# Kernel optimization log

Hardware: AMD Instinct MI355X
Metric: run time of the kernel (lower is better)

## Reference

```python
import jax, jax.numpy as jnp
import numpy as np
from jax import lax

EPS = 1e-5

def _conv(x, w, b, pad):
    y = lax.conv_general_dilated(x, w, (1, 1), [(pad, pad), (pad, pad)],
                                 dimension_numbers=('NCHW', 'OIHW', 'NCHW'))
    return y + b[None, :, None, None]

def _bn(x, g, b, m, v):
    # eval-mode BatchNorm2d with running stats
    scale = g * lax.rsqrt(v + EPS)
    return x * scale[None, :, None, None] + (b - m * scale)[None, :, None, None]

def setup_inputs() -> dict:
    key = jax.random.key(0)
    ks = jax.random.split(key, 16)
    B, C, H, W = 16, 64, 128, 128
    C2 = 2 * C
    d = {}
    d['x'] = jax.random.normal(ks[0], (B, C, H, W), jnp.float32)
    # fc1: Conv2d(C,C,3,p=1) + BN(C)
    d['fc1_w'] = jax.random.normal(ks[1], (C, C, 3, 3), jnp.float32) * 0.05
    d['fc1_b'] = jax.random.normal(ks[2], (C,), jnp.float32) * 0.05
    d['bn1_g'] = jnp.ones((C,), jnp.float32)
    d['bn1_b'] = jnp.zeros((C,), jnp.float32)
    d['bn1_m'] = jax.random.normal(ks[3], (C,), jnp.float32) * 0.05
    d['bn1_v'] = jax.random.uniform(ks[4], (C,), jnp.float32) * 0.5 + 0.5
    # graph_conv.nn: Conv2d(2C,2C,1) + BN(2C) + GELU
    d['gc_w'] = jax.random.normal(ks[5], (C2, C2, 1, 1), jnp.float32) * 0.05
    d['gc_b'] = jax.random.normal(ks[6], (C2,), jnp.float32) * 0.05
    d['bng_g'] = jnp.ones((C2,), jnp.float32)
    d['bng_b'] = jnp.zeros((C2,), jnp.float32)
    d['bng_m'] = jax.random.normal(ks[7], (C2,), jnp.float32) * 0.05
    d['bng_v'] = jax.random.uniform(ks[8], (C2,), jnp.float32) * 0.5 + 0.5
    # fc2: Conv2d(2C,C,3,p=1) + BN(C)
    d['fc2_w'] = jax.random.normal(ks[9], (C, C2, 3, 3), jnp.float32) * 0.05
    d['fc2_b'] = jax.random.normal(ks[10], (C,), jnp.float32) * 0.05
    d['bn2_g'] = jnp.ones((C,), jnp.float32)
    d['bn2_b'] = jnp.zeros((C,), jnp.float32)
    d['bn2_m'] = jax.random.normal(ks[11], (C,), jnp.float32) * 0.05
    d['bn2_v'] = jax.random.uniform(ks[12], (C,), jnp.float32) * 0.5 + 0.5
    return d

def reference(x, fc1_w, fc1_b, bn1_g, bn1_b, bn1_m, bn1_v,
              gc_w, gc_b, bng_g, bng_b, bng_m, bng_v,
              fc2_w, fc2_b, bn2_g, bn2_b, bn2_m, bn2_v):
    # fc1
    h = _bn(_conv(x, fc1_w, fc1_b, 1), bn1_g, bn1_b, bn1_m, bn1_v)
    # MRConv4dSP: strided self-attention over superpatch tokens
    sel = h[:, :, ::4, ::4]                          # [B,C,h4,w4]
    B, C, h4, w4 = sel.shape
    q = sel.reshape(B, C, h4 * w4).transpose(0, 2, 1)  # [B,N,C]
    scale = C ** (-0.5)
    att = jax.nn.softmax(jnp.einsum('bnc,bmc->bnm', q, q) * scale, axis=-1)
    o = jnp.einsum('bnm,bmc->bnc', att, q)           # [B,N,C]
    o = o.transpose(0, 2, 1).reshape(B, C, h4, w4)
    o = jnp.repeat(jnp.repeat(o, 4, axis=2), 4, axis=3)
    g = jnp.concatenate([h, o], axis=1)              # [B,2C,H,W]
    g = jax.nn.gelu(_bn(_conv(g, gc_w, gc_b, 0), bng_g, bng_b, bng_m, bng_v),
                    approximate=False)
    # fc2 + residual (drop_path=0 -> identity)
    y = _bn(_conv(g, fc2_w, fc2_b, 1), bn2_g, bn2_b, bn2_m, bn2_v)
    return y + x
```

## Files before the change

kernel.cpp:

```cpp
#include <hip/hip_runtime.h>
#include <math.h>

#define EPSV 1e-5f

typedef __bf16 bf16;
using bf16x8 = __attribute__((ext_vector_type(8))) __bf16;
using bf16x4 = __attribute__((ext_vector_type(4))) __bf16;
using bf16x2 = __attribute__((ext_vector_type(2))) __bf16;
using f32x4  = __attribute__((ext_vector_type(4))) float;

static __device__ __forceinline__ f32x4 mfma16(bf16x8 a, bf16x8 b, f32x4 c) {
    return __builtin_amdgcn_mfma_f32_16x16x32_bf16(a, b, c, 0, 0, 0);
}
static __device__ __forceinline__ f32x4 zero4() {
    f32x4 z = {0.f, 0.f, 0.f, 0.f};
    return z;
}
static __device__ __forceinline__ bf16x8 zero8() {
    bf16x8 z = {(bf16)0.f,(bf16)0.f,(bf16)0.f,(bf16)0.f,
                (bf16)0.f,(bf16)0.f,(bf16)0.f,(bf16)0.f};
    return z;
}

static __device__ __forceinline__ float gelu_f(float v) {
    float z = fabsf(v) * 0.70710678118f;
    float t = __builtin_amdgcn_rcpf(1.f + 0.3275911f * z);
    float poly = t * (0.254829592f + t * (-0.284496736f + t * (1.421413741f +
                 t * (-1.453152027f + t * 1.061405429f))));
    float e = __expf(-z * z);
    float erfv = copysignf(1.f - poly * e, v);
    return 0.5f * v * (1.f + erfv);
}

template<int CIN>
__global__ __launch_bounds__(256) void prep_conv_w(const float* __restrict__ w,
                                                   bf16* __restrict__ wt)
{
    int t = blockIdx.x * 256 + threadIdx.x;
    if (t >= 64 * CIN) return;
    int cout = t / CIN, ci = t - cout * CIN;
    int cci = ci >> 5, lg = (ci >> 3) & 3, j = ci & 7;
#pragma unroll
    for (int kgt = 0; kgt < 9; ++kgt) {
        float v = w[(size_t)t * 9 + kgt];
        wt[((((size_t)kgt * (CIN >> 5) + cci) * 4 + lg) * 64 + cout) * 8 + j] = (bf16)v;
    }
}

__global__ __launch_bounds__(256) void prep_1x1_w(const float* __restrict__ w,
                                                  bf16* __restrict__ wt)
{
    int t = blockIdx.x * 256 + threadIdx.x;
    int cout = t >> 7, ci = t & 127;
    int ks = ci >> 5, lg = (ci >> 3) & 3, j = ci & 7;
    wt[(((size_t)(ks * 4 + lg) * 128) + cout) * 8 + j] = (bf16)w[t];
}

__global__ __launch_bounds__(256) void cvt_x_nhwc(const float* __restrict__ x,
                                                  bf16* __restrict__ xb)
{
    __shared__ float t_lds[64 * 68];
    const int bx = blockIdx.x;
    const int b  = blockIdx.y;
    const int y  = bx >> 1, x0 = (bx & 1) * 64;
    const int tid = threadIdx.x;

    for (int f = tid; f < 64 * 16; f += 256) {
        int c = f >> 4, xu = f & 15;
        float4 v = *(const float4*)&x[((size_t)(b * 64 + c) << 14) + (y << 7) + x0 + xu * 4];
        t_lds[(xu * 4 + 0) * 68 + c] = v.x;
        t_lds[(xu * 4 + 1) * 68 + c] = v.y;
        t_lds[(xu * 4 + 2) * 68 + c] = v.z;
        t_lds[(xu * 4 + 3) * 68 + c] = v.w;
    }
    __syncthreads();
    for (int f = tid; f < 64 * 8; f += 256) {
        int xx = f >> 3, cu = f & 7;
        const float* p = &t_lds[xx * 68 + cu * 8];
        bf16x8 v;
#pragma unroll
        for (int j = 0; j < 8; ++j) v[j] = (bf16)p[j];
        *(bf16x8*)&xb[((size_t)((b * 128 + y) * 128) + x0 + xx) * 64 + cu * 8] = v;
    }
}

template<int CIN, int OUTMODE>
__global__ __launch_bounds__(512, 4) void conv3x3_mfma(
    const bf16* __restrict__ in, const bf16* __restrict__ wt,
    const float* __restrict__ bias,
    const float* __restrict__ bg, const float* __restrict__ bb,
    const float* __restrict__ bm, const float* __restrict__ bv,
    const float* __restrict__ resid, void* __restrict__ outp)
{
    constexpr int NC = CIN >> 5;
    __shared__ bf16 in_lds[10 * 34 * 40];

    const int tile = blockIdx.x;
    const int b    = blockIdx.y;
    const int x0 = (tile & 3) * 32;
    const int y0 = (tile >> 2) * 8;
    const int tid  = threadIdx.x;
    const int wid  = tid >> 6;
    const int lane = tid & 63;
    const int lix  = lane & 15, lg = lane >> 4;

    f32x4 acc[4][2];
#pragma unroll
    for (int i = 0; i < 4; ++i)
#pragma unroll
        for (int j = 0; j < 2; ++j) acc[i][j] = zero4();

    auto load_chunk = [&](int cci, bf16x8* pre) {
#pragma unroll
        for (int k = 0; k < 2; ++k) {
            int f = tid + k * 512;
            int u = f & 3, pix = f >> 2;
            int iy = pix / 34, ix = pix - iy * 34;
            int gy = y0 + iy - 1, gx = x0 + ix - 1;
            bf16x8 v = zero8();
            if ((unsigned)gy < 128u && (unsigned)gx < 128u)
                v = *(const bf16x8*)&in[((size_t)((b * 128 + gy) * 128 + gx)) * CIN + cci * 32 + u * 8];
            pre[k] = v;
        }
        {
            int f = 1024 + tid;
            int u = f & 3, pix = f >> 2;
            int iy = pix / 34, ix = pix - iy * 34;
            int gy = y0 + iy - 1, gx = x0 + ix - 1;
            bf16x8 v = zero8();
            if (tid < 336 && (unsigned)gy < 128u && (unsigned)gx < 128u)
                v = *(const bf16x8*)&in[((size_t)((b * 128 + gy) * 128 + gx)) * CIN + cci * 32 + u * 8];
            pre[2] = v;
        }
    };
    auto write_chunk = [&](const bf16x8* pre) {
#pragma unroll
        for (int k = 0; k < 2; ++k) {
            int f = tid + k * 512;
            int u = f & 3, pix = f >> 2;
            *(bf16x8*)&in_lds[pix * 40 + u * 8] = pre[k];
        }
        if (tid < 336) {
            int f = 1024 + tid;
            int u = f & 3, pix = f >> 2;
            *(bf16x8*)&in_lds[pix * 40 + u * 8] = pre[2];
        }
    };
    auto load_af = [&](int kgt, int cci, bf16x8* af) {
#pragma unroll
        for (int mi = 0; mi < 4; ++mi)
            af[mi] = *(const bf16x8*)&wt[((((size_t)kgt * NC + cci) * 4 + lg) * 64 + mi * 16 + lix) * 8];
    };
    auto compute = [&](int cci) {
        bf16x8 afA[4], afB[4];
        load_af(0, cci, afA);
#pragma unroll
        for (int kgt = 0; kgt < 9; ++kgt) {
            const int kg = kgt / 3, t = kgt % 3;
            bf16x8* cur = (kgt & 1) ? afB : afA;
            bf16x8* nxt = (kgt & 1) ? afA : afB;
            if (kgt < 8) load_af(kgt + 1, cci, nxt);
#pragma unroll
            for (int nj = 0; nj < 2; ++nj) {
                bf16x8 bfr = *(const bf16x8*)&in_lds[((wid + kg) * 34 + lix + t + nj * 16) * 40 + lg * 8];
#pragma unroll
                for (int mi = 0; mi < 4; ++mi)
                    acc[mi][nj] = mfma16(cur[mi], bfr, acc[mi][nj]);
            }
        }
    };

    bf16x8 preA[3], preB[3];
    load_chunk(0, preA);
#pragma unroll 1
    for (int cci = 0; cci < NC; cci += 2) {
        __syncthreads();
        write_chunk(preA);
        if (cci + 1 < NC) load_chunk(cci + 1, preB);
        __syncthreads();
        compute(cci);
        __syncthreads();
        write_chunk(preB);
        if (cci + 2 < NC) load_chunk(cci + 2, preA);
        __syncthreads();
        compute(cci + 1);
    }

    if (OUTMODE == 0) {
        bf16* out  = (bf16*)outp;
        bf16* stg  = in_lds;
#pragma unroll 1
        for (int p = 0; p < 2; ++p) {
            __syncthreads();
            if ((wid >> 2) == p) {
                int gyloc = wid & 3;
#pragma unroll
                for (int mi = 0; mi < 4; ++mi) {
                    float A[4], Bc[4];
#pragma unroll
                    for (int r = 0; r < 4; ++r) {
                        int c = mi * 16 + lg * 4 + r;
                        float s = bg[c] * rsqrtf(bv[c] + EPSV);
                        A[r]  = s;
                        Bc[r] = bias[c] * s + bb[c] - bm[c] * s;
                    }
#pragma unroll
                    for (int nj = 0; nj < 2; ++nj) {
                        int px = nj * 16 + lix;
                        bf16x4 vv;
#pragma unroll
                        for (int r = 0; r < 4; ++r)
                            vv[r] = (bf16)(acc[mi][nj][r] * A[r] + Bc[r]);
                        *(bf16x4*)&stg[(gyloc * 32 + px) * 68 + mi * 16 + lg * 4] = vv;
                    }
                }
            }
            __syncthreads();
#pragma unroll
            for (int k = 0; k < 2; ++k) {
                int idx = k * 512 + tid;
                int gyloc = idx >> 8, rem = idx & 255;
                int px = rem >> 3, cu = rem & 7;
                int gy = y0 + p * 4 + gyloc;
                bf16x8 v = *(const bf16x8*)&stg[(gyloc * 32 + px) * 68 + cu * 8];
                *(bf16x8*)&out[((size_t)((b * 128 + gy) * 128) + x0 + px) * 64 + cu * 8] = v;
            }
        }
    } else {
        float* out = (float*)outp;
        const int gy = y0 + wid;
#pragma unroll
        for (int mi = 0; mi < 4; ++mi) {
            float A[4], Bc[4];
#pragma unroll
            for (int r = 0; r < 4; ++r) {
                int c = mi * 16 + lg * 4 + r;
                float s = bg[c] * rsqrtf(bv[c] + EPSV);
                A[r]  = s;
                Bc[r] = bias[c] * s + bb[c] - bm[c] * s;
            }
#pragma unroll
            for (int nj = 0; nj < 2; ++nj) {
                int px = x0 + nj * 16 + lix;
#pragma unroll
                for (int r = 0; r < 4; ++r) {
                    int c = mi * 16 + lg * 4 + r;
                    size_t oi = ((size_t)(b * 64 + c) << 14) + (gy << 7) + px;
                    out[oi] = acc[mi][nj][r] * A[r] + Bc[r] + resid[oi];
                }
            }
        }
    }
}

__global__ __launch_bounds__(256) void gather_q(const bf16* __restrict__ h,
                                                bf16* __restrict__ q)
{
    int t = blockIdx.x * 256 + threadIdx.x;
    int cu = t & 7, n = (t >> 3) & 1023, b = t >> 13;
    int y = (n >> 5) << 2, x = (n & 31) << 2;
    bf16x8 v = *(const bf16x8*)&h[((size_t)((b * 128 + y) * 128 + x)) * 64 + cu * 8];
    *(bf16x8*)&q[((size_t)(b * 1024 + n)) * 64 + cu * 8] = v;
}

__global__ __launch_bounds__(256) void attn_fused(const bf16* __restrict__ q,
                                                  bf16* __restrict__ o)
{
    __shared__ bf16 qn[64 * 72];
    __shared__ bf16 kn[128 * 72];
    __shared__ bf16 vt[64 * 136];
    __shared__ bf16 pl[4][16 * 136];
    __shared__ __align__(16) float fac[4][16];
    const int n0 = blockIdx.x * 64, b = blockIdx.y;
    const int tid = threadIdx.x, w = tid >> 6, lane = tid & 63;
    const int lix = lane & 15, lg = lane >> 4;
    const bf16* qb = q + ((size_t)b << 16);

    for (int f = tid; f < 512; f += 256) {
        int row = f >> 3, cu = f & 7;
        *(bf16x8*)&qn[row * 72 + cu * 8] =
            *(const bf16x8*)&qb[(size_t)(n0 + row) * 64 + cu * 8];
    }

    float m_run = -3.0e38f, l_run = 0.f;
    f32x4 oacc[4];
#pragma unroll
    for (int ct = 0; ct < 4; ++ct) oacc[ct] = zero4();

    for (int mt = 0; mt < 1024; mt += 128) {
        __syncthreads();
        for (int f = tid; f < 1024; f += 256) {
            int row = f >> 3, cu = f & 7;
            *(bf16x8*)&kn[row * 72 + cu * 8] =
                *(const bf16x8*)&qb[(size_t)(mt + row) * 64 + cu * 8];
        }
        for (int f = tid; f < 512; f += 256) {
            int mp = f >> 3, cu = f & 7;
            int m = mp * 2;
            bf16x8 a = *(const bf16x8*)&qb[(size_t)(mt + m) * 64 + cu * 8];
            bf16x8 c = *(const bf16x8*)&qb[(size_t)(mt + m + 1) * 64 + cu * 8];
#pragma unroll
            for (int j = 0; j < 8; ++j) {
                bf16x2 pr = {a[j], c[j]};
                *(bf16x2*)&vt[(cu * 8 + j) * 136 + m] = pr;
            }
        }
        __syncthreads();

        bf16x8 bq0 = *(const bf16x8*)&qn[(w * 16 + lix) * 72 + lg * 8];
        bf16x8 bq1 = *(const bf16x8*)&qn[(w * 16 + lix) * 72 + 32 + lg * 8];

        f32x4 s[8];
#pragma unroll
        for (int t = 0; t < 8; ++t) {
            bf16x8 a0 = *(const bf16x8*)&kn[(t * 16 + lix) * 72 + lg * 8];
            bf16x8 a1 = *(const bf16x8*)&kn[(t * 16 + lix) * 72 + 32 + lg * 8];
            s[t] = mfma16(a0, bq0, zero4());
            s[t] = mfma16(a1, bq1, s[t]);
        }

        float mx = -3.0e38f;
#pragma unroll
        for (int t = 0; t < 8; ++t)
#pragma unroll
            for (int r = 0; r < 4; ++r) { s[t][r] *= 0.125f; mx = fmaxf(mx, s[t][r]); }
        mx = fmaxf(mx, __shfl_xor(mx, 16));
        mx = fmaxf(mx, __shfl_xor(mx, 32));
        float m_new = fmaxf(m_run, mx);
        float alpha = __expf(m_run - m_new);

        float psum = 0.f;
#pragma unroll
        for (int t = 0; t < 8; ++t) {
            float p0 = __expf(s[t][0] - m_new), p1 = __expf(s[t][1] - m_new);
            float p2 = __expf(s[t][2] - m_new), p3 = __expf(s[t][3] - m_new);
            psum += (p0 + p1) + (p2 + p3);
            bf16x2 v01 = {(bf16)p0, (bf16)p1};
            bf16x2 v23 = {(bf16)p2, (bf16)p3};
            *(bf16x2*)&pl[w][lix * 136 + t * 16 + lg * 4]     = v01;
            *(bf16x2*)&pl[w][lix * 136 + t * 16 + lg * 4 + 2] = v23;
        }
        psum += __shfl_xor(psum, 16);
        psum += __shfl_xor(psum, 32);
        l_run = l_run * alpha + psum;
        m_run = m_new;
        if (lg == 0) fac[w][lix] = alpha;

        float4 a4 = *(const float4*)&fac[w][lg * 4];
        float aa[4] = {a4.x, a4.y, a4.z, a4.w};
#pragma unroll
        for (int ct = 0; ct < 4; ++ct)
#pragma unroll
            for (int r = 0; r < 4; ++r) oacc[ct][r] *= aa[r];

#pragma unroll
        for (int kk = 0; kk < 4; ++kk) {
            bf16x8 pa = *(const bf16x8*)&pl[w][lix * 136 + kk * 32 + lg * 8];
#pragma unroll
            for (int ct = 0; ct < 4; ++ct) {
                bf16x8 bv = *(const bf16x8*)&vt[(ct * 16 + lix) * 136 + kk * 32 + lg * 8];
                oacc[ct] = mfma16(pa, bv, oacc[ct]);
            }
        }
    }

    if (lg == 0) fac[w][lix] = l_run;
    float4 l4 = *(const float4*)&fac[w][lg * 4];
    float ll[4] = {1.f / l4.x, 1.f / l4.y, 1.f / l4.z, 1.f / l4.w};
#pragma unroll
    for (int ct = 0; ct < 4; ++ct)
#pragma unroll
        for (int r = 0; r < 4; ++r) {
            int n = n0 + w * 16 + lg * 4 + r;
            int c = ct * 16 + lix;
            o[((size_t)(b * 1024 + n)) * 64 + c] = (bf16)(oacc[ct][r] * ll[r]);
        }
}

__global__ __launch_bounds__(256) void conv1x1_mfma(
    const bf16* __restrict__ h, const bf16* __restrict__ ov,
    const bf16* __restrict__ wt, const float* __restrict__ bias,
    const float* __restrict__ bg, const float* __restrict__ bb,
    const float* __restrict__ bm, const float* __restrict__ bv,
    bf16* __restrict__ g)
{
    __shared__ bf16 in1[128 * 136];
    const int y = blockIdx.x, b = blockIdx.y;
    const int tid = threadIdx.x;
    const int wid = tid >> 6, lane = tid & 63;
    const int lix = lane & 15, lg = lane >> 4;
    const int wm = wid >> 1, wn = wid & 1;

    for (int f = tid; f < 128 * 16; f += 256) {
        int px = f >> 4, cu = f & 15;
        bf16x8 v;
        if (cu < 8) {
            v = *(const bf16x8*)&h[((size_t)((b * 128 + y) * 128 + px)) * 64 + cu * 8];
        } else {
            int n = ((y >> 2) << 5) + (px >> 2);
            v = *(const bf16x8*)&ov[((size_t)(b * 1024 + n)) * 64 + (cu - 8) * 8];
        }
        *(bf16x8*)&in1[px * 136 + cu * 8] = v;
    }
    __syncthreads();

    f32x4 acc[4][4];
#pragma unroll
    for (int i = 0; i < 4; ++i)
#pragma unroll
        for (int j = 0; j < 4; ++j) acc[i][j] = zero4();

#pragma unroll
    for (int ks = 0; ks < 4; ++ks) {
        bf16x8 af[4], bfv[4];
#pragma unroll
        for (int mi = 0; mi < 4; ++mi)
            af[mi] = *(const bf16x8*)&wt[(((size_t)(ks * 4 + lg) * 128) + wm * 64 + mi * 16 + lix) * 8];
#pragma unroll
        for (int nj = 0; nj < 4; ++nj)
            bfv[nj] = *(const bf16x8*)&in1[(wn * 64 + nj * 16 + lix) * 136 + ks * 32 + lg * 8];
#pragma unroll
        for (int mi = 0; mi < 4; ++mi)
#pragma unroll
            for (int nj = 0; nj < 4; ++nj)
                acc[mi][nj] = mfma16(af[mi], bfv[nj], acc[mi][nj]);
    }

    __syncthreads();
    bf16* stg = in1;
#pragma unroll
    for (int mi = 0; mi < 4; ++mi) {
        float A[4], Bc[4];
#pragma unroll
        for (int r = 0; r < 4; ++r) {
            int c = wm * 64 + mi * 16 + lg * 4 + r;
            float s = bg[c] * rsqrtf(bv[c] + EPSV);
            A[r]  = s;
            Bc[r] = bias[c] * s + bb[c] - bm[c] * s;
        }
#pragma unroll
        for (int nj = 0; nj < 4; ++nj) {
            int px = wn * 64 + nj * 16 + lix;
            bf16x4 vv;
#pragma unroll
            for (int r = 0; r < 4; ++r)
                vv[r] = (bf16)gelu_f(acc[mi][nj][r] * A[r] + Bc[r]);
            *(bf16x4*)&stg[px * 132 + wm * 64 + mi * 16 + lg * 4] = vv;
        }
    }
    __syncthreads();
#pragma unroll
    for (int k = 0; k < 8; ++k) {
        int idx = k * 256 + tid;
        int px = idx >> 4, cu = idx & 15;
        bf16x8 v = *(const bf16x8*)&stg[px * 132 + cu * 8];
        *(bf16x8*)&g[((size_t)((b * 128 + y) * 128) + px) * 128 + cu * 8] = v;
    }
}

extern "C" void kernel_launch(void* const* d_in, const int* in_sizes, int n_in,
                              void* d_out, int out_size, void* d_ws, size_t ws_size,
                              hipStream_t stream)
{
    const float* x     = (const float*)d_in[0];
    const float* fc1_w = (const float*)d_in[1];
    const float* fc1_b = (const float*)d_in[2];
    const float* bn1_g = (const float*)d_in[3];
    const float* bn1_b = (const float*)d_in[4];
    const float* bn1_m = (const float*)d_in[5];
    const float* bn1_v = (const float*)d_in[6];
    const float* gc_w  = (const float*)d_in[7];
    const float* gc_b  = (const float*)d_in[8];
    const float* bng_g = (const float*)d_in[9];
    const float* bng_b = (const float*)d_in[10];
    const float* bng_m = (const float*)d_in[11];
    const float* bng_v = (const float*)d_in[12];
    const float* fc2_w = (const float*)d_in[13];
    const float* fc2_b = (const float*)d_in[14];
    const float* bn2_g = (const float*)d_in[15];
    const float* bn2_b = (const float*)d_in[16];
    const float* bn2_m = (const float*)d_in[17];
    const float* bn2_v = (const float*)d_in[18];

    char* wsb = (char*)d_ws;
    bf16* x_bf = (bf16*)wsb;
    bf16* h    = (bf16*)(wsb + 33554432);
    bf16* g    = (bf16*)(wsb + 67108864);
    bf16* q    = (bf16*)(wsb + 134217728);
    bf16* o    = (bf16*)(wsb + 136314880);
    bf16* wt1  = (bf16*)(wsb + 138412032);
    bf16* wt2  = (bf16*)(wsb + 138485760);
    bf16* wtg  = (bf16*)(wsb + 138633216);

    prep_conv_w<64><<<16, 256, 0, stream>>>(fc1_w, wt1);
    prep_conv_w<128><<<32, 256, 0, stream>>>(fc2_w, wt2);
    prep_1x1_w<<<64, 256, 0, stream>>>(gc_w, wtg);

    cvt_x_nhwc<<<dim3(256, 16), 256, 0, stream>>>(x, x_bf);

    conv3x3_mfma<64, 0><<<dim3(64, 16), 512, 0, stream>>>(
        x_bf, wt1, fc1_b, bn1_g, bn1_b, bn1_m, bn1_v, nullptr, h);

    gather_q<<<512, 256, 0, stream>>>(h, q);

    attn_fused<<<dim3(16, 16), 256, 0, stream>>>(q, o);

    conv1x1_mfma<<<dim3(128, 16), 256, 0, stream>>>(
        h, o, wtg, gc_b, bng_g, bng_b, bng_m, bng_v, g);

    conv3x3_mfma<128, 1><<<dim3(64, 16), 512, 0, stream>>>(
        g, wt2, fc2_b, bn2_g, bn2_b, bn2_m, bn2_v, x, (float*)d_out);
}
```

Measured before the change: 197.6 us.

## Retile conv3x3 to 4x64 output tiles with swizzled LDS and split channels

Changes the 3x3 conv tile from 8 rows by 32 columns to 4 rows by 64 columns. Each pair of waves now splits the 64 output channels in half and covers 64 pixels per row. The LDS layout drops the 40-element padding for a 32-wide XOR-swizzled layout, and global and LDS offsets are precomputed once outside the channel loop. The bf16 output path no longer stages through LDS and writes 4-element vectors straight to global memory. This aims to cut LDS bank conflicts, index arithmetic and halo overhead along x, but the taller halo fraction and narrower, less coalesced stores may offset that.

```diff
diff --git a/kernel.cpp b/kernel.cpp
--- a/kernel.cpp
+++ b/kernel.cpp
@@ -93,84 +93,84 @@
     const float* __restrict__ resid, void* __restrict__ outp)
 {
     constexpr int NC = CIN >> 5;
-    __shared__ bf16 in_lds[10 * 34 * 40];
+    __shared__ bf16 in_lds[6 * 66 * 32];
 
     const int tile = blockIdx.x;
     const int b    = blockIdx.y;
-    const int x0 = (tile & 3) * 32;
-    const int y0 = (tile >> 2) * 8;
+    const int x0 = (tile & 1) * 64;
+    const int y0 = (tile >> 1) * 4;
     const int tid  = threadIdx.x;
     const int wid  = tid >> 6;
     const int lane = tid & 63;
     const int lix  = lane & 15, lg = lane >> 4;
-
-    f32x4 acc[4][2];
-#pragma unroll
-    for (int i = 0; i < 4; ++i)
-#pragma unroll
-        for (int j = 0; j < 2; ++j) acc[i][j] = zero4();
+    const int rloc = wid >> 1;
+    const int ch   = wid & 1;
+
+    int goff[4], loff[4];
+    bool gok[4];
+#pragma unroll
+    for (int k = 0; k < 4; ++k) {
+        int f = k * 512 + tid;
+        int u = f & 3, pix = f >> 2;
+        int iy = pix / 66, ix = pix - iy * 66;
+        int gy = y0 + iy - 1, gx = x0 + ix - 1;
+        gok[k]  = (k < 3 || tid < 48) && (unsigned)gy < 128u && (unsigned)gx < 128u;
+        goff[k] = ((b * 128 + gy) * 128 + gx) * CIN + u * 8;
+        loff[k] = pix * 32 + ((u ^ (pix & 3)) << 3);
+    }
+    int rdbase[9];
+#pragma unroll
+    for (int kg = 0; kg < 3; ++kg)
+#pragma unroll
+        for (int t = 0; t < 3; ++t) {
+            int pix0 = (rloc + kg) * 66 + lix + t;
+            rdbase[kg * 3 + t] = pix0 * 32 + ((lg ^ (pix0 & 3)) << 3);
+        }
+
+    f32x4 acc[2][4];
+#pragma unroll
+    for (int i = 0; i < 2; ++i)
+#pragma unroll
+        for (int j = 0; j < 4; ++j) acc[i][j] = zero4();
 
     auto load_chunk = [&](int cci, bf16x8* pre) {
 #pragma unroll
-        for (int k = 0; k < 2; ++k) {
-            int f = tid + k * 512;
-            int u = f & 3, pix = f >> 2;
-            int iy = pix / 34, ix = pix - iy * 34;
-            int gy = y0 + iy - 1, gx = x0 + ix - 1;
+        for (int k = 0; k < 4; ++k) {
             bf16x8 v = zero8();
-            if ((unsigned)gy < 128u && (unsigned)gx < 128u)
-                v = *(const bf16x8*)&in[((size_t)((b * 128 + gy) * 128 + gx)) * CIN + cci * 32 + u * 8];
+            if (gok[k]) v = *(const bf16x8*)&in[goff[k] + cci * 32];
             pre[k] = v;
-        }
-        {
-            int f = 1024 + tid;
-            int u = f & 3, pix = f >> 2;
-            int iy = pix / 34, ix = pix - iy * 34;
-            int gy = y0 + iy - 1, gx = x0 + ix - 1;
-            bf16x8 v = zero8();
-            if (tid < 336 && (unsigned)gy < 128u && (unsigned)gx < 128u)
-                v = *(const bf16x8*)&in[((size_t)((b * 128 + gy) * 128 + gx)) * CIN + cci * 32 + u * 8];
-            pre[2] = v;
         }
     };
     auto write_chunk = [&](const bf16x8* pre) {
 #pragma unroll
-        for (int k = 0; k < 2; ++k) {
-            int f = tid + k * 512;
-            int u = f & 3, pix = f >> 2;
-            *(bf16x8*)&in_lds[pix * 40 + u * 8] = pre[k];
-        }
-        if (tid < 336) {
-            int f = 1024 + tid;
-            int u = f & 3, pix = f >> 2;
-            *(bf16x8*)&in_lds[pix * 40 + u * 8] = pre[2];
-        }
+        for (int k = 0; k < 3; ++k)
+            *(bf16x8*)&in_lds[loff[k]] = pre[k];
+        if (tid < 48) *(bf16x8*)&in_lds[loff[3]] = pre[3];
     };
     auto load_af = [&](int kgt, int cci, bf16x8* af) {
 #pragma unroll
-        for (int mi = 0; mi < 4; ++mi)
-            af[mi] = *(const bf16x8*)&wt[((((size_t)kgt * NC + cci) * 4 + lg) * 64 + mi * 16 + lix) * 8];
+        for (int mi = 0; mi < 2; ++mi)
+            af[mi] = *(const bf16x8*)&wt[((((size_t)kgt * NC + cci) * 4 + lg) * 64
+                                          + ch * 32 + mi * 16 + lix) * 8];
     };
     auto compute = [&](int cci) {
-        bf16x8 afA[4], afB[4];
+        bf16x8 afA[2], afB[2];
         load_af(0, cci, afA);
 #pragma unroll
         for (int kgt = 0; kgt < 9; ++kgt) {
-            const int kg = kgt / 3, t = kgt % 3;
             bf16x8* cur = (kgt & 1) ? afB : afA;
             bf16x8* nxt = (kgt & 1) ? afA : afB;
             if (kgt < 8) load_af(kgt + 1, cci, nxt);
 #pragma unroll
-            for (int nj = 0; nj < 2; ++nj) {
-                bf16x8 bfr = *(const bf16x8*)&in_lds[((wid + kg) * 34 + lix + t + nj * 16) * 40 + lg * 8];
-#pragma unroll
-                for (int mi = 0; mi < 4; ++mi)
-                    acc[mi][nj] = mfma16(cur[mi], bfr, acc[mi][nj]);
+            for (int nj = 0; nj < 4; ++nj) {
+                bf16x8 bfr = *(const bf16x8*)&in_lds[rdbase[kgt] + nj * 512];
+                acc[0][nj] = mfma16(cur[0], bfr, acc[0][nj]);
+                acc[1][nj] = mfma16(cur[1], bfr, acc[1][nj]);
             }
         }
     };
 
-    bf16x8 preA[3], preB[3];
+    bf16x8 preA[4], preB[4];
     load_chunk(0, preA);
 #pragma unroll 1
     for (int cci = 0; cci < NC; cci += 2) {
@@ -186,65 +186,37 @@
         compute(cci + 1);
     }
 
-    if (OUTMODE == 0) {
-        bf16* out  = (bf16*)outp;
-        bf16* stg  = in_lds;
-#pragma unroll 1
-        for (int p = 0; p < 2; ++p) {
-            __syncthreads();
-            if ((wid >> 2) == p) {
-                int gyloc = wid & 3;
-#pragma unroll
-                for (int mi = 0; mi < 4; ++mi) {
-                    float A[4], Bc[4];
-#pragma unroll
-                    for (int r = 0; r < 4; ++r) {
-                        int c = mi * 16 + lg * 4 + r;
-                        float s = bg[c] * rsqrtf(bv[c] + EPSV);
-                        A[r]  = s;
-                        Bc[r] = bias[c] * s + bb[c] - bm[c] * s;
-                    }
-#pragma unroll
-                    for (int nj = 0; nj < 2; ++nj) {
-                        int px = nj * 16 + lix;
-                        bf16x4 vv;
-#pragma unroll
-                        for (int r = 0; r < 4; ++r)
-                            vv[r] = (bf16)(acc[mi][nj][r] * A[r] + Bc[r]);
-                        *(bf16x4*)&stg[(gyloc * 32 + px) * 68 + mi * 16 + lg * 4] = vv;
-                    }
-                }
+    const int gy = y0 + rloc;
+#pragma unroll
+    for (int mi = 0; mi < 2; ++mi) {
+        float A[4], Bc[4];
+#pragma unroll
+        for (int r = 0; r < 4; ++r) {
+            int c = ch * 32 + mi * 16 + lg * 4 + r;
+            float s = bg[c] * rsqrtf(bv[c] + EPSV);
+            A[r]  = s;
+            Bc[r] = bias[c] * s + bb[c] - bm[c] * s;
+        }
+        if (OUTMODE == 0) {
+            bf16* out = (bf16*)outp;
+#pragma unroll
+            for (int nj = 0; nj < 4; ++nj) {
+                int px = x0 + nj * 16 + lix;
+                bf16x4 vv;
+#pragma unroll
+                for (int r = 0; r < 4; ++r)
+                    vv[r] = (bf16)(acc[mi][nj][r] * A[r] + Bc[r]);
+                *(bf16x4*)&out[((size_t)((b * 128 + gy) * 128) + px) * 64
+                               + ch * 32 + mi * 16 + lg * 4] = vv;
             }
-            __syncthreads();
-#pragma unroll
-            for (int k = 0; k < 2; ++k) {
-                int idx = k * 512 + tid;
-                int gyloc = idx >> 8, rem = idx & 255;
-                int px = rem >> 3, cu = rem & 7;
-                int gy = y0 + p * 4 + gyloc;
-                bf16x8 v = *(const bf16x8*)&stg[(gyloc * 32 + px) * 68 + cu * 8];
-                *(bf16x8*)&out[((size_t)((b * 128 + gy) * 128) + x0 + px) * 64 + cu * 8] = v;
-            }
-        }
-    } else {
-        float* out = (float*)outp;
-        const int gy = y0 + wid;
-#pragma unroll
-        for (int mi = 0; mi < 4; ++mi) {
-            float A[4], Bc[4];
-#pragma unroll
-            for (int r = 0; r < 4; ++r) {
-                int c = mi * 16 + lg * 4 + r;
-                float s = bg[c] * rsqrtf(bv[c] + EPSV);
-                A[r]  = s;
-                Bc[r] = bias[c] * s + bb[c] - bm[c] * s;
-            }
-#pragma unroll
-            for (int nj = 0; nj < 2; ++nj) {
+        } else {
+            float* out = (float*)outp;
+#pragma unroll
+            for (int nj = 0; nj < 4; ++nj) {
                 int px = x0 + nj * 16 + lix;
 #pragma unroll
                 for (int r = 0; r < 4; ++r) {
-                    int c = mi * 16 + lg * 4 + r;
+                    int c = ch * 32 + mi * 16 + lg * 4 + r;
                     size_t oi = ((size_t)(b * 64 + c) << 14) + (gy << 7) + px;
                     out[oi] = acc[mi][nj][r] * A[r] + Bc[r] + resid[oi];
                 }
```

Result: slower. 201.6 us (+2.0%).
